# Kernel tuning notes

Hardware: AMD Instinct MI355X
Metric: run time of the kernel (lower is better)

Reference implementation:

```python
import math
import jax, jax.numpy as jnp
import numpy as np

B, L, D_MODEL = 2, 2048, 1024
N_HEAD, HEAD_DIM = 16, 64
ATT_SCALE = 1.0  # divisor is sqrt(head_dim ** attention_scale)


def setup_inputs() -> dict:
    key = jax.random.key(0)
    ks = jax.random.split(key, 6)
    HD = N_HEAD * HEAD_DIM
    # Xavier-uniform style init for projection weights (stored as [in, out])
    def xavier(k, fan_in, fan_out):
        lim = math.sqrt(6.0 / (fan_in + fan_out))
        return jax.random.uniform(k, (fan_in, fan_out), jnp.float32, -lim, lim)
    return {
        "x":  jax.random.normal(ks[0], (B, L, D_MODEL), jnp.float32),
        "Wq": xavier(ks[1], D_MODEL, HD), "bq": jnp.zeros((HD,), jnp.float32),
        "Wk": xavier(ks[2], D_MODEL, HD), "bk": jnp.zeros((HD,), jnp.float32),
        "Wv": xavier(ks[3], D_MODEL, HD), "bv": jnp.zeros((HD,), jnp.float32),
        "Wo": xavier(ks[4], HD, D_MODEL),
        "bo": jax.random.uniform(ks[5], (D_MODEL,), jnp.float32, -1.0 / math.sqrt(HD), 1.0 / math.sqrt(HD)),
    }


def reference(x, Wq, bq, Wk, bk, Wv, bv, Wo, bo):
    b, l, _ = x.shape
    # QKV projections -> [B, L, H, Dh]
    q = (x @ Wq + bq).reshape(b, l, N_HEAD, HEAD_DIM)
    k = (x @ Wk + bk).reshape(b, l, N_HEAD, HEAD_DIM)
    v = (x @ Wv + bv).reshape(b, l, N_HEAD, HEAD_DIM)
    scale = 1.0 / math.sqrt(HEAD_DIM ** ATT_SCALE)
    # Unnormalized (no softmax) attention: (Q K^T / sqrt(Dh)) V
    scores = jnp.einsum("blhd,bmhd->bhlm", q, k) * scale  # [B,H,L,L]
    attn = jnp.einsum("bhlm,bmhd->blhd", scores, v)        # [B,L,H,Dh]
    out = attn.reshape(b, l, N_HEAD * HEAD_DIM) @ Wo + bo  # dispatcher
    return out
```

## Files before the change

### kernel.cpp

```cpp
#include <hip/hip_runtime.h>
#include <stdint.h>

#define B_ 2
#define L_ 2048
#define DM 1024
#define NH 16
#define DH 64
#define M_ (B_*L_)
#define NQKV 3072

typedef short short8 __attribute__((ext_vector_type(8)));
typedef float f32x4 __attribute__((ext_vector_type(4)));

__device__ __forceinline__ unsigned short f2b(float f) {
    union { float f; unsigned int u; } v; v.f = f;
    unsigned int u = v.u;
    return (unsigned short)((u + 0x7fffu + ((u >> 16) & 1u)) >> 16);
}

__device__ __forceinline__ void gld_lds16(const void* g, void* l) {
    __builtin_amdgcn_global_load_lds(
        (const __attribute__((address_space(1))) void*)g,
        (__attribute__((address_space(3))) void*)l, 16, 0, 0);
}

__global__ __launch_bounds__(256)
void setup_kernel(const float* __restrict__ x,
                  const float* __restrict__ Wq, const float* __restrict__ Wk,
                  const float* __restrict__ Wv, const float* __restrict__ Wo,
                  const float* __restrict__ bq, const float* __restrict__ bk,
                  const float* __restrict__ bv,
                  unsigned short* __restrict__ xb, unsigned short* __restrict__ WqkvT,
                  unsigned short* __restrict__ WoT, float* __restrict__ biasq,
                  float* __restrict__ KtV)
{
    __shared__ float tile[32][33];
    const int bid = blockIdx.x;
    const int t = threadIdx.x;

    if (bid < 2048) {
        int i = (bid * 256 + t) * 8;
        float4 a0 = *(const float4*)(x + i);
        float4 a1 = *(const float4*)(x + i + 4);
        uint4 p;
        p.x = (unsigned)f2b(a0.x) | ((unsigned)f2b(a0.y) << 16);
        p.y = (unsigned)f2b(a0.z) | ((unsigned)f2b(a0.w) << 16);
        p.z = (unsigned)f2b(a1.x) | ((unsigned)f2b(a1.y) << 16);
        p.w = (unsigned)f2b(a1.z) | ((unsigned)f2b(a1.w) << 16);
        *(uint4*)(xb + i) = p;
    } else if (bid < 2048 + 4096) {
        int wb = bid - 2048;
        int wi = wb >> 10;
        int tid = wb & 1023;
        const float* W = (wi == 0) ? Wq : (wi == 1) ? Wk : (wi == 2) ? Wv : Wo;
        unsigned short* dst = (wi < 3) ? (WqkvT + (size_t)wi * 1024 * 1024) : WoT;
        int n0 = (tid & 31) * 32, k0 = (tid >> 5) * 32;
        int r = t >> 3, c4 = (t & 7) << 2;
        float4 v = *(const float4*)(W + (size_t)(k0 + r) * DM + n0 + c4);
        tile[r][c4+0] = v.x; tile[r][c4+1] = v.y; tile[r][c4+2] = v.z; tile[r][c4+3] = v.w;
        __syncthreads();
        uint2 o;
        o.x = (unsigned)f2b(tile[c4+0][r]) | ((unsigned)f2b(tile[c4+1][r]) << 16);
        o.y = (unsigned)f2b(tile[c4+2][r]) | ((unsigned)f2b(tile[c4+3][r]) << 16);
        *(uint2*)(dst + (size_t)(n0 + r) * DM + k0 + c4) = o;
    } else if (bid < 2048 + 4096 + 12) {
        int i = (bid - 6144) * 256 + t;
        float v = (i < 1024) ? bq[i] : (i < 2048 ? bk[i - 1024] : bv[i - 2048]);
        biasq[i] = v;
    } else {
        int i = ((bid - 6156) * 256 + t) * 4;
        float4 z; z.x = z.y = z.z = z.w = 0.f;
        *(float4*)(KtV + i) = z;
    }
}

template<int BN, bool OUT_BF16>
__global__ __launch_bounds__(256)
void gemm_tn_kernel(const unsigned short* __restrict__ A,
                    const unsigned short* __restrict__ Bt,
                    const float* __restrict__ bias,
                    void* __restrict__ C,
                    int M, int N, int K)
{
    constexpr int BM = 128, BK = 64;
    constexpr int MI = (BN == 128) ? 4 : 2;
    constexpr int MJ = 4;
    __shared__ __align__(16) unsigned short As[BM * BK];
    __shared__ __align__(16) unsigned short Bs[BN * BK];

    const int t = threadIdx.x;
    const int w = t >> 6, lane = t & 63;
    const int quad = lane >> 4, l16 = lane & 15;
    const int wm = (BN == 128) ? (w >> 1) : w;
    const int wn = (BN == 128) ? (w & 1) : 0;
    const int m0 = blockIdx.y * BM, n0 = blockIdx.x * BN;

    f32x4 acc[MI][MJ];
    #pragma unroll
    for (int i = 0; i < MI; i++)
        #pragma unroll
        for (int j = 0; j < MJ; j++)
            #pragma unroll
            for (int r = 0; r < 4; r++) acc[i][j][r] = 0.f;

    for (int kk = 0; kk < K; kk += BK) {
        #pragma unroll
        for (int p = 0; p < 4; p++) {
            int c = p * 256 + t;
            int row = c >> 3, slot = c & 7;
            int g = slot ^ ((row >> 1) & 7);
            gld_lds16(A + (size_t)(m0 + row) * K + kk + g * 8,
                      (char*)As + p * 4096 + w * 1024);
        }
        #pragma unroll
        for (int p = 0; p < BN / 32; p++) {
            int c = p * 256 + t;
            int row = c >> 3, slot = c & 7;
            int g = slot ^ ((row >> 1) & 7);
            gld_lds16(Bt + (size_t)(n0 + row) * K + kk + g * 8,
                      (char*)Bs + p * 4096 + w * 1024);
        }
        __syncthreads();

        #pragma unroll
        for (int ks = 0; ks < 2; ks++) {
            int kc = ks * 4 + quad;
            short8 afr[MI], bfr[MJ];
            #pragma unroll
            for (int i = 0; i < MI; i++) {
                int am = wm * (MI * 16) + i * 16 + l16;
                afr[i] = *(const short8*)((const char*)As + am * 128 + ((kc ^ ((am >> 1) & 7)) << 4));
            }
            #pragma unroll
            for (int j = 0; j < MJ; j++) {
                int bn = wn * 64 + j * 16 + l16;
                bfr[j] = *(const short8*)((const char*)Bs + bn * 128 + ((kc ^ ((bn >> 1) & 7)) << 4));
            }
            #pragma unroll
            for (int i = 0; i < MI; i++)
                #pragma unroll
                for (int j = 0; j < MJ; j++)
                    acc[i][j] = __builtin_amdgcn_mfma_f32_16x16x32_bf16(afr[i], bfr[j], acc[i][j], 0, 0, 0);
        }
        __syncthreads();
    }

    #pragma unroll
    for (int j = 0; j < MJ; j++) {
        int col = n0 + wn * 64 + j * 16 + l16;
        float bv = bias[col];
        #pragma unroll
        for (int i = 0; i < MI; i++) {
            #pragma unroll
            for (int r = 0; r < 4; r++) {
                int row = m0 + wm * (MI * 16) + i * 16 + quad * 4 + r;
                float v = acc[i][j][r] + bv;
                if constexpr (OUT_BF16)
                    ((unsigned short*)C)[(size_t)row * N + col] = f2b(v);
                else
                    ((float*)C)[(size_t)row * N + col] = v;
            }
        }
    }
}


__global__ __launch_bounds__(256)
void ktv_mfma_kernel(const unsigned short* __restrict__ QKV, float* __restrict__ KtV)
{
    __shared__ __align__(16) unsigned short Ksl[64][40];
    __shared__ __align__(16) unsigned short Vsl[64][40];

    const int bh = blockIdx.x, chunk = blockIdx.y;
    const int b = bh >> 4, h = bh & 15;
    const int t = threadIdx.x;
    const int wave = t >> 6, lane = t & 63;
    const int quad = lane >> 4, l16 = lane & 15;
    const int lrow = t >> 3, c0 = (t & 7) << 3;

    f32x4 acc[4];
    #pragma unroll
    for (int i = 0; i < 4; i++)
        #pragma unroll
        for (int r = 0; r < 4; r++) acc[i][r] = 0.f;

    const size_t base0 = ((size_t)(b * L_ + chunk * 128)) * NQKV + (size_t)h * DH;
    for (int kk = 0; kk < 128; kk += 32) {
        size_t rb = base0 + (size_t)(kk + lrow) * NQKV + c0;
        uint4 kp = *(const uint4*)(QKV + rb + 1024);
        uint4 vp = *(const uint4*)(QKV + rb + 2048);
        Ksl[c0+0][lrow] = (unsigned short)(kp.x & 0xffff);
        Ksl[c0+1][lrow] = (unsigned short)(kp.x >> 16);
        Ksl[c0+2][lrow] = (unsigned short)(kp.y & 0xffff);
        Ksl[c0+3][lrow] = (unsigned short)(kp.y >> 16);
        Ksl[c0+4][lrow] = (unsigned short)(kp.z & 0xffff);
        Ksl[c0+5][lrow] = (unsigned short)(kp.z >> 16);
        Ksl[c0+6][lrow] = (unsigned short)(kp.w & 0xffff);
        Ksl[c0+7][lrow] = (unsigned short)(kp.w >> 16);
        Vsl[c0+0][lrow] = (unsigned short)(vp.x & 0xffff);
        Vsl[c0+1][lrow] = (unsigned short)(vp.x >> 16);
        Vsl[c0+2][lrow] = (unsigned short)(vp.y & 0xffff);
        Vsl[c0+3][lrow] = (unsigned short)(vp.y >> 16);
        Vsl[c0+4][lrow] = (unsigned short)(vp.z & 0xffff);
        Vsl[c0+5][lrow] = (unsigned short)(vp.z >> 16);
        Vsl[c0+6][lrow] = (unsigned short)(vp.w & 0xffff);
        Vsl[c0+7][lrow] = (unsigned short)(vp.w >> 16);
        __syncthreads();

        short8 af = *(const short8*)&Ksl[wave * 16 + l16][quad * 8];
        #pragma unroll
        for (int nt = 0; nt < 4; nt++) {
            short8 bfr = *(const short8*)&Vsl[nt * 16 + l16][quad * 8];
            acc[nt] = __builtin_amdgcn_mfma_f32_16x16x32_bf16(af, bfr, acc[nt], 0, 0, 0);
        }
        __syncthreads();
    }

    float* dst0 = KtV + (size_t)bh * 64 * 64;
    #pragma unroll
    for (int nt = 0; nt < 4; nt++) {
        int col = nt * 16 + l16;
        #pragma unroll
        for (int r = 0; r < 4; r++) {
            int row = wave * 16 + quad * 4 + r;
            atomicAdd(dst0 + row * 64 + col, acc[nt][r] * 0.125f);
        }
    }
}

__global__ __launch_bounds__(256)
void qktv_mfma_kernel(const unsigned short* __restrict__ QKV, const float* __restrict__ KtV,
                      unsigned short* __restrict__ attn)
{
    __shared__ __align__(16) unsigned short Qsl[64][72];
    __shared__ __align__(16) unsigned short Bsl[64][72];

    const int bh = blockIdx.x, mt = blockIdx.y;
    const int b = bh >> 4, h = bh & 15;
    const int t = threadIdx.x;
    const int wave = t >> 6, lane = t & 63;
    const int quad = lane >> 4, l16 = lane & 15;
    const int m0 = b * L_ + mt * 64;
    const int row = t >> 2, c0 = (t & 3) << 4;

    const unsigned short* qp = QKV + (size_t)(m0 + row) * NQKV + h * DH + c0;
    *(uint4*)&Qsl[row][c0]     = *(const uint4*)qp;
    *(uint4*)&Qsl[row][c0 + 8] = *(const uint4*)(qp + 8);

    const float* kp = KtV + ((size_t)bh * 64 + row) * 64 + c0;
    #pragma unroll
    for (int j = 0; j < 16; j++) Bsl[c0 + j][row] = f2b(kp[j]);
    __syncthreads();

    f32x4 acc[4];
    #pragma unroll
    for (int i = 0; i < 4; i++)
        #pragma unroll
        for (int r = 0; r < 4; r++) acc[i][r] = 0.f;

    #pragma unroll
    for (int ks = 0; ks < 2; ks++) {
        short8 af = *(const short8*)&Qsl[wave * 16 + l16][ks * 32 + quad * 8];
        #pragma unroll
        for (int nt = 0; nt < 4; nt++) {
            short8 bfr = *(const short8*)&Bsl[nt * 16 + l16][ks * 32 + quad * 8];
            acc[nt] = __builtin_amdgcn_mfma_f32_16x16x32_bf16(af, bfr, acc[nt], 0, 0, 0);
        }
    }

    #pragma unroll
    for (int nt = 0; nt < 4; nt++) {
        int col = h * DH + nt * 16 + l16;
        #pragma unroll
        for (int r = 0; r < 4; r++) {
            int grow = m0 + wave * 16 + quad * 4 + r;
            attn[(size_t)grow * DM + col] = f2b(acc[nt][r]);
        }
    }
}


extern "C" void kernel_launch(void* const* d_in, const int* in_sizes, int n_in,
                              void* d_out, int out_size, void* d_ws, size_t ws_size,
                              hipStream_t stream)
{
    const float* x  = (const float*)d_in[0];
    const float* Wq = (const float*)d_in[1];
    const float* bq = (const float*)d_in[2];
    const float* Wk = (const float*)d_in[3];
    const float* bk = (const float*)d_in[4];
    const float* Wv = (const float*)d_in[5];
    const float* bv = (const float*)d_in[6];
    const float* Wo = (const float*)d_in[7];
    const float* bo = (const float*)d_in[8];

    char* ws = (char*)d_ws;
    unsigned short* xb    = (unsigned short*)(ws);
    unsigned short* WqkvT = (unsigned short*)(ws + (size_t)8  * 1024 * 1024);
    unsigned short* WoT   = (unsigned short*)(ws + (size_t)14 * 1024 * 1024);
    float*          biasq = (float*)         (ws + (size_t)16 * 1024 * 1024);
    unsigned short* QKV   = (unsigned short*)(ws + (size_t)17 * 1024 * 1024);
    float*          KtV   = (float*)         (ws + (size_t)41 * 1024 * 1024);
    unsigned short* attn  = xb;

    setup_kernel<<<6284, 256, 0, stream>>>(x, Wq, Wk, Wv, Wo, bq, bk, bv,
                                           xb, WqkvT, WoT, biasq, KtV);

    gemm_tn_kernel<128, true><<<dim3(NQKV / 128, M_ / 128), 256, 0, stream>>>(
        xb, WqkvT, biasq, QKV, M_, NQKV, DM);

    ktv_mfma_kernel<<<dim3(B_ * NH, 16), 256, 0, stream>>>(QKV, KtV);
    qktv_mfma_kernel<<<dim3(B_ * NH, L_ / 64), 256, 0, stream>>>(QKV, KtV, attn);

    gemm_tn_kernel<64, false><<<dim3(DM / 64, M_ / 128), 256, 0, stream>>>(
        attn, WoT, bo, d_out, M_, DM, DM);
}
```

Before: 167.6 us.

## Fold KtV into output projection weights, replacing per-row attention GEMM

```diff
diff --git a/kernel.cpp b/kernel.cpp
--- a/kernel.cpp
+++ b/kernel.cpp
@@ -74,19 +74,19 @@
     }
 }
 
-template<int BN, bool OUT_BF16>
+template<int BN, bool OUT_BF16, bool BATCHED_B>
 __global__ __launch_bounds__(256)
-void gemm_tn_kernel(const unsigned short* __restrict__ A,
+void gemm_tn_kernel(const unsigned short* __restrict__ A, int lda,
                     const unsigned short* __restrict__ Bt,
                     const float* __restrict__ bias,
                     void* __restrict__ C,
                     int M, int N, int K)
 {
-    constexpr int BM = 128, BK = 64;
+    constexpr int BM = 128;
     constexpr int MI = (BN == 128) ? 4 : 2;
     constexpr int MJ = 4;
-    __shared__ __align__(16) unsigned short As[BM * BK];
-    __shared__ __align__(16) unsigned short Bs[BN * BK];
+    __shared__ __align__(16) unsigned short As[BM * 32];
+    __shared__ __align__(16) unsigned short Bs[BN * 32];
 
     const int t = threadIdx.x;
     const int w = t >> 6, lane = t & 63;
@@ -95,6 +95,8 @@
     const int wn = (BN == 128) ? (w & 1) : 0;
     const int m0 = blockIdx.y * BM, n0 = blockIdx.x * BN;
 
+    if constexpr (BATCHED_B) Bt += (size_t)(m0 >> 11) * 1024 * 1024;
+
     f32x4 acc[MI][MJ];
     #pragma unroll
     for (int i = 0; i < MI; i++)
@@ -103,45 +105,42 @@
             #pragma unroll
             for (int r = 0; r < 4; r++) acc[i][j][r] = 0.f;
 
-    for (int kk = 0; kk < K; kk += BK) {
-        #pragma unroll
-        for (int p = 0; p < 4; p++) {
-            int c = p * 256 + t;
-            int row = c >> 3, slot = c & 7;
-            int g = slot ^ ((row >> 1) & 7);
-            gld_lds16(A + (size_t)(m0 + row) * K + kk + g * 8,
+    const int srow = t >> 2;
+    const int schunk = t & 3;
+
+    for (int kk = 0; kk < K; kk += 32) {
+        #pragma unroll
+        for (int p = 0; p < 2; p++) {
+            int row = p * 64 + srow;
+            int g = schunk ^ ((row >> 1) & 3);
+            gld_lds16(A + (size_t)(m0 + row) * lda + kk + g * 8,
                       (char*)As + p * 4096 + w * 1024);
         }
         #pragma unroll
-        for (int p = 0; p < BN / 32; p++) {
-            int c = p * 256 + t;
-            int row = c >> 3, slot = c & 7;
-            int g = slot ^ ((row >> 1) & 7);
+        for (int p = 0; p < BN / 64; p++) {
+            int row = p * 64 + srow;
+            int g = schunk ^ ((row >> 1) & 3);
             gld_lds16(Bt + (size_t)(n0 + row) * K + kk + g * 8,
                       (char*)Bs + p * 4096 + w * 1024);
         }
         __syncthreads();
 
-        #pragma unroll
-        for (int ks = 0; ks < 2; ks++) {
-            int kc = ks * 4 + quad;
-            short8 afr[MI], bfr[MJ];
+        short8 afr[MI], bfr[MJ];
+        #pragma unroll
+        for (int i = 0; i < MI; i++) {
+            int am = wm * (MI * 16) + i * 16 + l16;
+            afr[i] = *(const short8*)((const char*)As + am * 64 + ((quad ^ ((am >> 1) & 3)) << 4));
+        }
+        #pragma unroll
+        for (int j = 0; j < MJ; j++) {
+            int bn = wn * 64 + j * 16 + l16;
+            bfr[j] = *(const short8*)((const char*)Bs + bn * 64 + ((quad ^ ((bn >> 1) & 3)) << 4));
+        }
+        #pragma unroll
+        for (int i = 0; i < MI; i++)
             #pragma unroll
-            for (int i = 0; i < MI; i++) {
-                int am = wm * (MI * 16) + i * 16 + l16;
-                afr[i] = *(const short8*)((const char*)As + am * 128 + ((kc ^ ((am >> 1) & 7)) << 4));
-            }
-            #pragma unroll
-            for (int j = 0; j < MJ; j++) {
-                int bn = wn * 64 + j * 16 + l16;
-                bfr[j] = *(const short8*)((const char*)Bs + bn * 128 + ((kc ^ ((bn >> 1) & 7)) << 4));
-            }
-            #pragma unroll
-            for (int i = 0; i < MI; i++)
-                #pragma unroll
-                for (int j = 0; j < MJ; j++)
-                    acc[i][j] = __builtin_amdgcn_mfma_f32_16x16x32_bf16(afr[i], bfr[j], acc[i][j], 0, 0, 0);
-        }
+            for (int j = 0; j < MJ; j++)
+                acc[i][j] = __builtin_amdgcn_mfma_f32_16x16x32_bf16(afr[i], bfr[j], acc[i][j], 0, 0, 0);
         __syncthreads();
     }
 
@@ -229,27 +228,27 @@
 }
 
 __global__ __launch_bounds__(256)
-void qktv_mfma_kernel(const unsigned short* __restrict__ QKV, const float* __restrict__ KtV,
-                      unsigned short* __restrict__ attn)
-{
-    __shared__ __align__(16) unsigned short Qsl[64][72];
+void zmat_kernel(const unsigned short* __restrict__ WoT, const float* __restrict__ KtV,
+                 unsigned short* __restrict__ ZT)
+{
+    __shared__ __align__(16) unsigned short Asl[64][72];
     __shared__ __align__(16) unsigned short Bsl[64][72];
 
-    const int bh = blockIdx.x, mt = blockIdx.y;
+    const int bh = blockIdx.x, nt0 = blockIdx.y;
     const int b = bh >> 4, h = bh & 15;
     const int t = threadIdx.x;
     const int wave = t >> 6, lane = t & 63;
     const int quad = lane >> 4, l16 = lane & 15;
-    const int m0 = b * L_ + mt * 64;
+    const int n0 = nt0 * 64;
     const int row = t >> 2, c0 = (t & 3) << 4;
 
-    const unsigned short* qp = QKV + (size_t)(m0 + row) * NQKV + h * DH + c0;
-    *(uint4*)&Qsl[row][c0]     = *(const uint4*)qp;
-    *(uint4*)&Qsl[row][c0 + 8] = *(const uint4*)(qp + 8);
+    const unsigned short* ap = WoT + (size_t)(n0 + row) * DM + h * DH + c0;
+    *(uint4*)&Asl[row][c0]     = *(const uint4*)ap;
+    *(uint4*)&Asl[row][c0 + 8] = *(const uint4*)(ap + 8);
 
     const float* kp = KtV + ((size_t)bh * 64 + row) * 64 + c0;
     #pragma unroll
-    for (int j = 0; j < 16; j++) Bsl[c0 + j][row] = f2b(kp[j]);
+    for (int j = 0; j < 16; j++) Bsl[row][c0 + j] = f2b(kp[j]);
     __syncthreads();
 
     f32x4 acc[4];
@@ -260,7 +259,7 @@
 
     #pragma unroll
     for (int ks = 0; ks < 2; ks++) {
-        short8 af = *(const short8*)&Qsl[wave * 16 + l16][ks * 32 + quad * 8];
+        short8 af = *(const short8*)&Asl[wave * 16 + l16][ks * 32 + quad * 8];
         #pragma unroll
         for (int nt = 0; nt < 4; nt++) {
             short8 bfr = *(const short8*)&Bsl[nt * 16 + l16][ks * 32 + quad * 8];
@@ -268,13 +267,14 @@
         }
     }
 
+    unsigned short* zb = ZT + (size_t)b * 1024 * 1024 + (size_t)h * DH;
     #pragma unroll
     for (int nt = 0; nt < 4; nt++) {
-        int col = h * DH + nt * 16 + l16;
+        int col = nt * 16 + l16;
         #pragma unroll
         for (int r = 0; r < 4; r++) {
-            int grow = m0 + wave * 16 + quad * 4 + r;
-            attn[(size_t)grow * DM + col] = f2b(acc[nt][r]);
+            int zr = n0 + wave * 16 + quad * 4 + r;
+            zb[(size_t)zr * 1024 + col] = f2b(acc[nt][r]);
         }
     }
 }
@@ -301,17 +301,18 @@
     float*          biasq = (float*)         (ws + (size_t)16 * 1024 * 1024);
     unsigned short* QKV   = (unsigned short*)(ws + (size_t)17 * 1024 * 1024);
     float*          KtV   = (float*)         (ws + (size_t)41 * 1024 * 1024);
-    unsigned short* attn  = xb;
+    unsigned short* ZT    = xb;
 
     setup_kernel<<<6284, 256, 0, stream>>>(x, Wq, Wk, Wv, Wo, bq, bk, bv,
                                            xb, WqkvT, WoT, biasq, KtV);
 
-    gemm_tn_kernel<128, true><<<dim3(NQKV / 128, M_ / 128), 256, 0, stream>>>(
-        xb, WqkvT, biasq, QKV, M_, NQKV, DM);
+    gemm_tn_kernel<128, true, false><<<dim3(NQKV / 128, M_ / 128), 256, 0, stream>>>(
+        xb, DM, WqkvT, biasq, QKV, M_, NQKV, DM);
 
     ktv_mfma_kernel<<<dim3(B_ * NH, 16), 256, 0, stream>>>(QKV, KtV);
-    qktv_mfma_kernel<<<dim3(B_ * NH, L_ / 64), 256, 0, stream>>>(QKV, KtV, attn);
-
-    gemm_tn_kernel<64, false><<<dim3(DM / 64, M_ / 128), 256, 0, stream>>>(
-        attn, WoT, bo, d_out, M_, DM, DM);
-}
+
+    zmat_kernel<<<dim3(B_ * NH, 16), 256, 0, stream>>>(WoT, KtV, ZT);
+
+    gemm_tn_kernel<64, false, true><<<dim3(DM / 64, M_ / 128), 256, 0, stream>>>(
+        QKV, NQKV, ZT, bo, d_out, M_, DM, DM);
+}
```

Result: no change. 164.8 us (-1.7%).
